# Optimization experiments

Hardware: AMD Instinct MI355X
Metric: run time of the kernel (lower is better)

The kernel has to match this reference:

```python
import jax, jax.numpy as jnp
import numpy as np

N_NODES = 50000
N_EDGES = 800000
NUM_FEATURES = 96
HIDDEN = 96


def _glorot(key, fan_in, fan_out):
    s = np.sqrt(6.0 / (fan_in + fan_out)).astype(np.float32)
    return jax.random.uniform(key, (fan_in, fan_out), minval=-s, maxval=s, dtype=jnp.float32)


def setup_inputs() -> dict:
    key = jax.random.key(0)
    ks = jax.random.split(key, 8)
    x = jax.random.normal(ks[0], (N_NODES, NUM_FEATURES), dtype=jnp.float32)
    edge_index = jax.random.randint(ks[1], (2, N_EDGES), 0, N_NODES, dtype=jnp.int64)
    return {
        "x": x,
        "W1": _glorot(ks[2], NUM_FEATURES, HIDDEN),
        "b1": jnp.zeros((HIDDEN,), jnp.float32),
        "W2": _glorot(ks[3], HIDDEN, HIDDEN),
        "b2": jnp.zeros((HIDDEN,), jnp.float32),
        "W3": _glorot(ks[4], HIDDEN, HIDDEN),
        "b3": jnp.zeros((HIDDEN,), jnp.float32),
        "edge_index": edge_index,
    }


def _gcn_conv(x, src, dst, W, b):
    """PyG GCNConv: add self-loops, symmetric normalization D^-1/2 (A+I) D^-1/2 X W + b."""
    n = x.shape[0]
    h = x @ W  # [N, H]
    # degree with self-loops (in-degree over dst, +1 for the self-loop)
    deg = jax.ops.segment_sum(jnp.ones_like(dst, dtype=h.dtype), dst, num_segments=n) + 1.0
    dinv = jax.lax.rsqrt(deg)  # [N]
    norm = dinv[src] * dinv[dst]  # [E]
    # scatter normalized messages; self-loop contributes h_i / deg_i
    agg = jax.ops.segment_sum(h[src] * norm[:, None], dst, num_segments=n)
    return agg + h * (dinv * dinv)[:, None] + b


def reference(x, W1, b1, W2, b2, W3, b3, edge_index):
    src, dst = edge_index[0], edge_index[1]
    # dropout is a no-op in eval mode (F.dropout with training=False)
    h = jax.nn.relu(_gcn_conv(x, src, dst, W1, b1))
    h = jax.nn.relu(_gcn_conv(h, src, dst, W2, b2))
    return _gcn_conv(h, src, dst, W3, b3)
```

## Files before the change

### kernel.cpp

```cpp
#include <hip/hip_runtime.h>

#define F 96
#define SCAN_B 1024

#define WT_IDX(c, k) ((c) * 96 + (((k) ^ (((c) & 7) << 2))))


__global__ void k_zero_i(int* __restrict__ p, int n) {
    int i = blockIdx.x * blockDim.x + threadIdx.x;
    if (i < n) p[i] = 0;
}

__global__ void k_hist(const int* __restrict__ dst, int* __restrict__ hist, int E) {
    int e = blockIdx.x * blockDim.x + threadIdx.x;
    if (e < E) atomicAdd(&hist[dst[e]], 1);
}

__global__ void k_dinv(const int* __restrict__ hist, float* __restrict__ dinv, int N) {
    int i = blockIdx.x * blockDim.x + threadIdx.x;
    if (i < N) dinv[i] = rsqrtf((float)hist[i] + 1.0f);
}

__global__ __launch_bounds__(SCAN_B) void k_scan1(const int* __restrict__ hist,
                                                  int* __restrict__ incl,
                                                  int* __restrict__ bsum, int N) {
    __shared__ int s[SCAN_B];
    int i = blockIdx.x * SCAN_B + threadIdx.x;
    int v = (i < N) ? hist[i] : 0;
    s[threadIdx.x] = v;
    __syncthreads();
    for (int off = 1; off < SCAN_B; off <<= 1) {
        int add = (threadIdx.x >= off) ? s[threadIdx.x - off] : 0;
        __syncthreads();
        s[threadIdx.x] += add;
        __syncthreads();
    }
    if (i < N) incl[i] = s[threadIdx.x];
    if (threadIdx.x == SCAN_B - 1) bsum[blockIdx.x] = s[SCAN_B - 1];
}

__global__ __launch_bounds__(SCAN_B) void k_scan2(int* __restrict__ bsum, int nb) {
    __shared__ int s[SCAN_B];
    int v = (threadIdx.x < nb) ? bsum[threadIdx.x] : 0;
    s[threadIdx.x] = v;
    __syncthreads();
    for (int off = 1; off < SCAN_B; off <<= 1) {
        int add = (threadIdx.x >= off) ? s[threadIdx.x - off] : 0;
        __syncthreads();
        s[threadIdx.x] += add;
        __syncthreads();
    }
    if (threadIdx.x < nb) bsum[threadIdx.x] = s[threadIdx.x] - v;
}

__global__ void k_scan3(const int* __restrict__ incl, const int* __restrict__ hist,
                        const int* __restrict__ bsum, int* __restrict__ row_ptr,
                        int* __restrict__ cursor, int N, int E) {
    int i = blockIdx.x * blockDim.x + threadIdx.x;
    if (i < N) {
        int start = incl[i] - hist[i] + bsum[i / SCAN_B];
        row_ptr[i] = start;
        cursor[i] = start;
    }
    if (i == 0) row_ptr[N] = E;
}

__global__ void k_place(const int* __restrict__ src, const int* __restrict__ dst,
                        int* __restrict__ cursor, int* __restrict__ csr_src, int E) {
    int e = blockIdx.x * blockDim.x + threadIdx.x;
    if (e >= E) return;
    int pos = atomicAdd(&cursor[dst[e]], 1);
    csr_src[pos] = src[e];
}


template <bool RELU_IN>
__global__ __launch_bounds__(256) void k_dense(const float* __restrict__ X,
                                               const float* __restrict__ W,
                                               float* __restrict__ H, int N) {
    __shared__ float Wt[96 * 96];
    __shared__ float Xs[64][96];
    int t = threadIdx.x;
    for (int i = t; i < F * F; i += 256) {
        int k = i / F, c = i % F;
        Wt[WT_IDX(c, k)] = W[i];
    }
    int row0 = blockIdx.x * 64;
    for (int i = t; i < 64 * 24; i += 256) {
        int r = i / 24, c4 = (i % 24) * 4;
        int gr = row0 + r;
        float4 v = make_float4(0.f, 0.f, 0.f, 0.f);
        if (gr < N) {
            v = *reinterpret_cast<const float4*>(X + (size_t)gr * F + c4);
            if (RELU_IN) {
                v.x = fmaxf(v.x, 0.f); v.y = fmaxf(v.y, 0.f);
                v.z = fmaxf(v.z, 0.f); v.w = fmaxf(v.w, 0.f);
            }
        }
        *reinterpret_cast<float4*>(&Xs[r][c4]) = v;
    }
    __syncthreads();

    int c2 = t & 31;
    int rg = t >> 5;
    float acc[8][3];
#pragma unroll
    for (int j = 0; j < 8; ++j) { acc[j][0] = 0.f; acc[j][1] = 0.f; acc[j][2] = 0.f; }

    for (int k4 = 0; k4 < F; k4 += 4) {
        float4 w0 = *reinterpret_cast<const float4*>(&Wt[WT_IDX(c2, k4)]);
        float4 w1 = *reinterpret_cast<const float4*>(&Wt[WT_IDX(c2 + 32, k4)]);
        float4 w2 = *reinterpret_cast<const float4*>(&Wt[WT_IDX(c2 + 64, k4)]);
#pragma unroll
        for (int j = 0; j < 8; ++j) {
            float4 xv = *reinterpret_cast<const float4*>(&Xs[rg + 8 * j][k4]);
            acc[j][0] = fmaf(xv.x, w0.x, acc[j][0]);
            acc[j][1] = fmaf(xv.x, w1.x, acc[j][1]);
            acc[j][2] = fmaf(xv.x, w2.x, acc[j][2]);
            acc[j][0] = fmaf(xv.y, w0.y, acc[j][0]);
            acc[j][1] = fmaf(xv.y, w1.y, acc[j][1]);
            acc[j][2] = fmaf(xv.y, w2.y, acc[j][2]);
            acc[j][0] = fmaf(xv.z, w0.z, acc[j][0]);
            acc[j][1] = fmaf(xv.z, w1.z, acc[j][1]);
            acc[j][2] = fmaf(xv.z, w2.z, acc[j][2]);
            acc[j][0] = fmaf(xv.w, w0.w, acc[j][0]);
            acc[j][1] = fmaf(xv.w, w1.w, acc[j][1]);
            acc[j][2] = fmaf(xv.w, w2.w, acc[j][2]);
        }
    }

#pragma unroll
    for (int j = 0; j < 8; ++j) {
        int gr = row0 + rg + 8 * j;
        if (gr < N) {
            float* hp = H + (size_t)gr * F;
            hp[c2]      = acc[j][0];
            hp[c2 + 32] = acc[j][1];
            hp[c2 + 64] = acc[j][2];
        }
    }
}


__global__ __launch_bounds__(256) void k_gather(const float* __restrict__ H,
                                                const int* __restrict__ csr_src,
                                                const int* __restrict__ row_ptr,
                                                const float* __restrict__ dinv,
                                                const float* __restrict__ b,
                                                float* __restrict__ O, int N) {
    int t = blockIdx.x * 256 + threadIdx.x;
    int node = t >> 5;
    if (node >= N) return;
    int lf = t & 31;
    int s0 = row_ptr[node], s1 = row_ptr[node + 1];
    float di = dinv[node];
    float d2 = di * di;
    const float* hn = H + (size_t)node * F;
    float a0 = fmaf(hn[lf],      d2, b[lf]);
    float a1 = fmaf(hn[lf + 32], d2, b[lf + 32]);
    float a2 = fmaf(hn[lf + 64], d2, b[lf + 64]);

    int e = s0;
    for (; e + 3 < s1; e += 4) {
        int sA = csr_src[e],     sB = csr_src[e + 1];
        int sC = csr_src[e + 2], sD = csr_src[e + 3];
        float wA = dinv[sA] * di, wB = dinv[sB] * di;
        float wC = dinv[sC] * di, wD = dinv[sD] * di;
        const float* hA = H + (size_t)sA * F;
        const float* hB = H + (size_t)sB * F;
        const float* hC = H + (size_t)sC * F;
        const float* hD = H + (size_t)sD * F;
        a0 = fmaf(hA[lf], wA, a0); a1 = fmaf(hA[lf + 32], wA, a1); a2 = fmaf(hA[lf + 64], wA, a2);
        a0 = fmaf(hB[lf], wB, a0); a1 = fmaf(hB[lf + 32], wB, a1); a2 = fmaf(hB[lf + 64], wB, a2);
        a0 = fmaf(hC[lf], wC, a0); a1 = fmaf(hC[lf + 32], wC, a1); a2 = fmaf(hC[lf + 64], wC, a2);
        a0 = fmaf(hD[lf], wD, a0); a1 = fmaf(hD[lf + 32], wD, a1); a2 = fmaf(hD[lf + 64], wD, a2);
    }
    for (; e < s1; ++e) {
        int sA = csr_src[e];
        float wA = dinv[sA] * di;
        const float* hA = H + (size_t)sA * F;
        a0 = fmaf(hA[lf], wA, a0);
        a1 = fmaf(hA[lf + 32], wA, a1);
        a2 = fmaf(hA[lf + 64], wA, a2);
    }

    float* o = O + (size_t)node * F;
    o[lf]      = a0;
    o[lf + 32] = a1;
    o[lf + 64] = a2;
}


__global__ void k_init_deg(float* __restrict__ deg, int N) {
    int i = blockIdx.x * blockDim.x + threadIdx.x;
    if (i < N) deg[i] = 1.0f;
}
__global__ void k_count(const int* __restrict__ dst, float* __restrict__ deg, int E) {
    int e = blockIdx.x * blockDim.x + threadIdx.x;
    if (e < E) atomicAdd(&deg[dst[e]], 1.0f);
}
__global__ void k_rsqrt(float* __restrict__ deg, int N) {
    int i = blockIdx.x * blockDim.x + threadIdx.x;
    if (i < N) deg[i] = rsqrtf(deg[i]);
}
__global__ void k_init_out(const float* __restrict__ H, const float* __restrict__ dinv,
                           const float* __restrict__ b, float* __restrict__ O, int N) {
    int idx = blockIdx.x * blockDim.x + threadIdx.x;
    if (idx >= N * F) return;
    int i = idx / F, f = idx % F;
    float di = dinv[i];
    O[idx] = fmaf(H[idx], di * di, b[f]);
}
__global__ __launch_bounds__(256) void k_scatter(const float* __restrict__ H,
                                                 const int* __restrict__ src,
                                                 const int* __restrict__ dst,
                                                 const float* __restrict__ dinv,
                                                 float* __restrict__ O, int E) {
    int t = blockIdx.x * 256 + threadIdx.x;
    int e = t >> 5;
    if (e >= E) return;
    int lf = t & 31;
    int s = src[e], d = dst[e];
    float nrm = dinv[s] * dinv[d];
    const float* hs = H + (size_t)s * F;
    float* od = O + (size_t)d * F;
#pragma unroll
    for (int j = 0; j < 3; ++j) atomicAdd(&od[lf + 32 * j], hs[lf + 32 * j] * nrm);
}


extern "C" void kernel_launch(void* const* d_in, const int* in_sizes, int n_in,
                              void* d_out, int out_size, void* d_ws, size_t ws_size,
                              hipStream_t stream) {
    const float* x  = (const float*)d_in[0];
    const float* W1 = (const float*)d_in[1];
    const float* b1 = (const float*)d_in[2];
    const float* W2 = (const float*)d_in[3];
    const float* b2 = (const float*)d_in[4];
    const float* W3 = (const float*)d_in[5];
    const float* b3 = (const float*)d_in[6];
    const int*   ei = (const int*)d_in[7];

    const int N = in_sizes[0] / F;
    const int E = in_sizes[7] / 2;
    const int* src = ei;
    const int* dst = ei + E;
    const size_t NF = (size_t)N * F;

    const int thr = 256;
    dim3 blk(thr);
    int gN  = (N + thr - 1) / thr;
    int gE  = (E + thr - 1) / thr;
    int gDen = (N + 63) / 64;
    int gGat = (int)(((size_t)N * 32 + thr - 1) / thr);
    int nScanB = (N + SCAN_B - 1) / SCAN_B;

    float* dinv    = (float*)d_ws;
    int*   row_ptr = (int*)(dinv + N);
    int*   csr_src = row_ptr + N + 1;
    float* A       = (float*)(csr_src + E);
    float* B       = A + NF;
    int* hist   = (int*)A;
    int* incl   = hist + N;
    int* cursor = (int*)B;
    int* bsum   = cursor + N;

    size_t need = ((size_t)N + (N + 1) + (size_t)E + 2 * NF) * 4;
    float* out = (float*)d_out;

    if (ws_size >= need && nScanB <= SCAN_B) {
        k_zero_i<<<gN, blk, 0, stream>>>(hist, N);
        k_hist<<<gE, blk, 0, stream>>>(dst, hist, E);
        k_scan1<<<nScanB, dim3(SCAN_B), 0, stream>>>(hist, incl, bsum, N);
        k_scan2<<<1, dim3(SCAN_B), 0, stream>>>(bsum, nScanB);
        k_scan3<<<gN, blk, 0, stream>>>(incl, hist, bsum, row_ptr, cursor, N, E);
        k_dinv<<<gN, blk, 0, stream>>>(hist, dinv, N);
        k_place<<<gE, blk, 0, stream>>>(src, dst, cursor, csr_src, E);

        k_dense<false><<<gDen, blk, 0, stream>>>(x, W1, A, N);
        k_gather<<<gGat, blk, 0, stream>>>(A, csr_src, row_ptr, dinv, b1, B, N);
        k_dense<true><<<gDen, blk, 0, stream>>>(B, W2, A, N);
        k_gather<<<gGat, blk, 0, stream>>>(A, csr_src, row_ptr, dinv, b2, B, N);
        k_dense<true><<<gDen, blk, 0, stream>>>(B, W3, A, N);
        k_gather<<<gGat, blk, 0, stream>>>(A, csr_src, row_ptr, dinv, b3, out, N);
    } else {
        float* fdinv = (float*)d_ws;
        float* fA = fdinv + N;
        float* fB = fA + NF;
        int gNF = (int)((NF + thr - 1) / thr);
        int gSc = (int)(((size_t)E * 32 + thr - 1) / thr);
        k_init_deg<<<gN, blk, 0, stream>>>(fdinv, N);
        k_count<<<gE, blk, 0, stream>>>(dst, fdinv, E);
        k_rsqrt<<<gN, blk, 0, stream>>>(fdinv, N);
        k_dense<false><<<gDen, blk, 0, stream>>>(x, W1, fA, N);
        k_init_out<<<gNF, blk, 0, stream>>>(fA, fdinv, b1, fB, N);
        k_scatter<<<gSc, blk, 0, stream>>>(fA, src, dst, fdinv, fB, E);
        k_dense<true><<<gDen, blk, 0, stream>>>(fB, W2, fA, N);
        k_init_out<<<gNF, blk, 0, stream>>>(fA, fdinv, b2, out, N);
        k_scatter<<<gSc, blk, 0, stream>>>(fA, src, dst, fdinv, out, E);
        k_dense<true><<<gDen, blk, 0, stream>>>(out, W3, fA, N);
        k_init_out<<<gNF, blk, 0, stream>>>(fA, fdinv, b3, fB, N);
        k_scatter<<<gSc, blk, 0, stream>>>(fA, src, dst, fdinv, fB, E);
        hipMemcpyAsync(out, fB, NF * sizeof(float), hipMemcpyDeviceToDevice, stream);
    }
}
```

Baseline: 360.9 us.

## Store hidden features in feature-chunked layout and gather per chunk with one thread per node

The dense kernel now writes H as 8 column chunks of 12 features each, every chunk stored contiguously for all nodes. The gather kernel assigns one thread per node per chunk and reads 48-byte vectors, so each chunk's working set is N*48 bytes, which should fit in cache better than the full 384-byte rows. Blocks interleave chunks so that chunks of the same node range run concurrently. Index and output accesses use nontemporal loads and stores. In exchange, the dense stores become scattered, csr_src and dinv are reread once per chunk, and one thread per node may cause load imbalance on high-degree nodes.

```diff
diff --git a/kernel.cpp b/kernel.cpp
--- a/kernel.cpp
+++ b/kernel.cpp
@@ -2,6 +2,10 @@
 
 #define F 96
 #define SCAN_B 1024
+#define CHUNKS 8
+#define CW 12
+
+typedef float f32x4 __attribute__((ext_vector_type(4)));
 
 #define WT_IDX(c, k) ((c) * 96 + (((k) ^ (((c) & 7) << 2))))
 
@@ -74,7 +78,7 @@
 }
 
 
-template <bool RELU_IN>
+template <bool RELU_IN, bool CHUNKED>
 __global__ __launch_bounds__(256) void k_dense(const float* __restrict__ X,
                                                const float* __restrict__ W,
                                                float* __restrict__ H, int N) {
@@ -129,65 +133,111 @@
         }
     }
 
+    size_t NC = (size_t)N * CW;
 #pragma unroll
     for (int j = 0; j < 8; ++j) {
         int gr = row0 + rg + 8 * j;
         if (gr < N) {
-            float* hp = H + (size_t)gr * F;
-            hp[c2]      = acc[j][0];
-            hp[c2 + 32] = acc[j][1];
-            hp[c2 + 64] = acc[j][2];
+            if (CHUNKED) {
+#pragma unroll
+                for (int m = 0; m < 3; ++m) {
+                    int c = c2 + 32 * m;
+                    H[(size_t)(c / CW) * NC + (size_t)gr * CW + (c % CW)] = acc[j][m];
+                }
+            } else {
+                float* hp = H + (size_t)gr * F;
+                hp[c2]      = acc[j][0];
+                hp[c2 + 32] = acc[j][1];
+                hp[c2 + 64] = acc[j][2];
+            }
         }
     }
 }
 
 
-__global__ __launch_bounds__(256) void k_gather(const float* __restrict__ H,
+__global__ __launch_bounds__(256) void k_gather(const float* __restrict__ Hc,
                                                 const int* __restrict__ csr_src,
                                                 const int* __restrict__ row_ptr,
                                                 const float* __restrict__ dinv,
                                                 const float* __restrict__ b,
                                                 float* __restrict__ O, int N) {
-    int t = blockIdx.x * 256 + threadIdx.x;
-    int node = t >> 5;
+    int chunk = blockIdx.x & (CHUNKS - 1);
+    int node = (blockIdx.x >> 3) * 256 + threadIdx.x;
     if (node >= N) return;
-    int lf = t & 31;
-    int s0 = row_ptr[node], s1 = row_ptr[node + 1];
+    size_t NC = (size_t)N * CW;
+    const float* Hk = Hc + (size_t)chunk * NC;
+
+    int s0 = __builtin_nontemporal_load(row_ptr + node);
+    int s1 = __builtin_nontemporal_load(row_ptr + node + 1);
     float di = dinv[node];
     float d2 = di * di;
-    const float* hn = H + (size_t)node * F;
-    float a0 = fmaf(hn[lf],      d2, b[lf]);
-    float a1 = fmaf(hn[lf + 32], d2, b[lf + 32]);
-    float a2 = fmaf(hn[lf + 64], d2, b[lf + 64]);
+
+    const float* bc = b + chunk * CW;
+    const float* hn = Hk + (size_t)node * CW;
+    float4 a0 = *reinterpret_cast<const float4*>(bc);
+    float4 a1 = *reinterpret_cast<const float4*>(bc + 4);
+    float4 a2 = *reinterpret_cast<const float4*>(bc + 8);
+    {
+        float4 h0 = *reinterpret_cast<const float4*>(hn);
+        float4 h1 = *reinterpret_cast<const float4*>(hn + 4);
+        float4 h2 = *reinterpret_cast<const float4*>(hn + 8);
+        a0.x = fmaf(h0.x, d2, a0.x); a0.y = fmaf(h0.y, d2, a0.y);
+        a0.z = fmaf(h0.z, d2, a0.z); a0.w = fmaf(h0.w, d2, a0.w);
+        a1.x = fmaf(h1.x, d2, a1.x); a1.y = fmaf(h1.y, d2, a1.y);
+        a1.z = fmaf(h1.z, d2, a1.z); a1.w = fmaf(h1.w, d2, a1.w);
+        a2.x = fmaf(h2.x, d2, a2.x); a2.y = fmaf(h2.y, d2, a2.y);
+        a2.z = fmaf(h2.z, d2, a2.z); a2.w = fmaf(h2.w, d2, a2.w);
+    }
 
     int e = s0;
-    for (; e + 3 < s1; e += 4) {
-        int sA = csr_src[e],     sB = csr_src[e + 1];
-        int sC = csr_src[e + 2], sD = csr_src[e + 3];
-        float wA = dinv[sA] * di, wB = dinv[sB] * di;
-        float wC = dinv[sC] * di, wD = dinv[sD] * di;
-        const float* hA = H + (size_t)sA * F;
-        const float* hB = H + (size_t)sB * F;
-        const float* hC = H + (size_t)sC * F;
-        const float* hD = H + (size_t)sD * F;
-        a0 = fmaf(hA[lf], wA, a0); a1 = fmaf(hA[lf + 32], wA, a1); a2 = fmaf(hA[lf + 64], wA, a2);
-        a0 = fmaf(hB[lf], wB, a0); a1 = fmaf(hB[lf + 32], wB, a1); a2 = fmaf(hB[lf + 64], wB, a2);
-        a0 = fmaf(hC[lf], wC, a0); a1 = fmaf(hC[lf + 32], wC, a1); a2 = fmaf(hC[lf + 64], wC, a2);
-        a0 = fmaf(hD[lf], wD, a0); a1 = fmaf(hD[lf + 32], wD, a1); a2 = fmaf(hD[lf + 64], wD, a2);
-    }
-    for (; e < s1; ++e) {
-        int sA = csr_src[e];
+    for (; e + 1 < s1; e += 2) {
+        int sA = __builtin_nontemporal_load(csr_src + e);
+        int sB = __builtin_nontemporal_load(csr_src + e + 1);
         float wA = dinv[sA] * di;
-        const float* hA = H + (size_t)sA * F;
-        a0 = fmaf(hA[lf], wA, a0);
-        a1 = fmaf(hA[lf + 32], wA, a1);
-        a2 = fmaf(hA[lf + 64], wA, a2);
-    }
-
-    float* o = O + (size_t)node * F;
-    o[lf]      = a0;
-    o[lf + 32] = a1;
-    o[lf + 64] = a2;
+        float wB = dinv[sB] * di;
+        const float* hA = Hk + (size_t)sA * CW;
+        const float* hB = Hk + (size_t)sB * CW;
+        float4 A0 = *reinterpret_cast<const float4*>(hA);
+        float4 A1 = *reinterpret_cast<const float4*>(hA + 4);
+        float4 A2 = *reinterpret_cast<const float4*>(hA + 8);
+        float4 B0 = *reinterpret_cast<const float4*>(hB);
+        float4 B1 = *reinterpret_cast<const float4*>(hB + 4);
+        float4 B2 = *reinterpret_cast<const float4*>(hB + 8);
+        a0.x = fmaf(A0.x, wA, a0.x); a0.y = fmaf(A0.y, wA, a0.y);
+        a0.z = fmaf(A0.z, wA, a0.z); a0.w = fmaf(A0.w, wA, a0.w);
+        a1.x = fmaf(A1.x, wA, a1.x); a1.y = fmaf(A1.y, wA, a1.y);
+        a1.z = fmaf(A1.z, wA, a1.z); a1.w = fmaf(A1.w, wA, a1.w);
+        a2.x = fmaf(A2.x, wA, a2.x); a2.y = fmaf(A2.y, wA, a2.y);
+        a2.z = fmaf(A2.z, wA, a2.z); a2.w = fmaf(A2.w, wA, a2.w);
+        a0.x = fmaf(B0.x, wB, a0.x); a0.y = fmaf(B0.y, wB, a0.y);
+        a0.z = fmaf(B0.z, wB, a0.z); a0.w = fmaf(B0.w, wB, a0.w);
+        a1.x = fmaf(B1.x, wB, a1.x); a1.y = fmaf(B1.y, wB, a1.y);
+        a1.z = fmaf(B1.z, wB, a1.z); a1.w = fmaf(B1.w, wB, a1.w);
+        a2.x = fmaf(B2.x, wB, a2.x); a2.y = fmaf(B2.y, wB, a2.y);
+        a2.z = fmaf(B2.z, wB, a2.z); a2.w = fmaf(B2.w, wB, a2.w);
+    }
+    if (e < s1) {
+        int sA = __builtin_nontemporal_load(csr_src + e);
+        float wA = dinv[sA] * di;
+        const float* hA = Hk + (size_t)sA * CW;
+        float4 A0 = *reinterpret_cast<const float4*>(hA);
+        float4 A1 = *reinterpret_cast<const float4*>(hA + 4);
+        float4 A2 = *reinterpret_cast<const float4*>(hA + 8);
+        a0.x = fmaf(A0.x, wA, a0.x); a0.y = fmaf(A0.y, wA, a0.y);
+        a0.z = fmaf(A0.z, wA, a0.z); a0.w = fmaf(A0.w, wA, a0.w);
+        a1.x = fmaf(A1.x, wA, a1.x); a1.y = fmaf(A1.y, wA, a1.y);
+        a1.z = fmaf(A1.z, wA, a1.z); a1.w = fmaf(A1.w, wA, a1.w);
+        a2.x = fmaf(A2.x, wA, a2.x); a2.y = fmaf(A2.y, wA, a2.y);
+        a2.z = fmaf(A2.z, wA, a2.z); a2.w = fmaf(A2.w, wA, a2.w);
+    }
+
+    float* o = O + (size_t)node * F + chunk * CW;
+    f32x4 v0 = {a0.x, a0.y, a0.z, a0.w};
+    f32x4 v1 = {a1.x, a1.y, a1.z, a1.w};
+    f32x4 v2 = {a2.x, a2.y, a2.z, a2.w};
+    __builtin_nontemporal_store(v0, (f32x4*)o);
+    __builtin_nontemporal_store(v1, (f32x4*)(o + 4));
+    __builtin_nontemporal_store(v2, (f32x4*)(o + 8));
 }
 
 
@@ -252,7 +302,7 @@
     int gN  = (N + thr - 1) / thr;
     int gE  = (E + thr - 1) / thr;
     int gDen = (N + 63) / 64;
-    int gGat = (int)(((size_t)N * 32 + thr - 1) / thr);
+    int gGat = CHUNKS * ((N + thr - 1) / thr);
     int nScanB = (N + SCAN_B - 1) / SCAN_B;
 
     float* dinv    = (float*)d_ws;
@@ -277,11 +327,11 @@
         k_dinv<<<gN, blk, 0, stream>>>(hist, dinv, N);
         k_place<<<gE, blk, 0, stream>>>(src, dst, cursor, csr_src, E);
 
-        k_dense<false><<<gDen, blk, 0, stream>>>(x, W1, A, N);
+        k_dense<false, true><<<gDen, blk, 0, stream>>>(x, W1, A, N);
         k_gather<<<gGat, blk, 0, stream>>>(A, csr_src, row_ptr, dinv, b1, B, N);
-        k_dense<true><<<gDen, blk, 0, stream>>>(B, W2, A, N);
+        k_dense<true, true><<<gDen, blk, 0, stream>>>(B, W2, A, N);
         k_gather<<<gGat, blk, 0, stream>>>(A, csr_src, row_ptr, dinv, b2, B, N);
-        k_dense<true><<<gDen, blk, 0, stream>>>(B, W3, A, N);
+        k_dense<true, true><<<gDen, blk, 0, stream>>>(B, W3, A, N);
         k_gather<<<gGat, blk, 0, stream>>>(A, csr_src, row_ptr, dinv, b3, out, N);
     } else {
         float* fdinv = (float*)d_ws;
@@ -292,13 +342,13 @@
         k_init_deg<<<gN, blk, 0, stream>>>(fdinv, N);
         k_count<<<gE, blk, 0, stream>>>(dst, fdinv, E);
         k_rsqrt<<<gN, blk, 0, stream>>>(fdinv, N);
-        k_dense<false><<<gDen, blk, 0, stream>>>(x, W1, fA, N);
+        k_dense<false, false><<<gDen, blk, 0, stream>>>(x, W1, fA, N);
         k_init_out<<<gNF, blk, 0, stream>>>(fA, fdinv, b1, fB, N);
         k_scatter<<<gSc, blk, 0, stream>>>(fA, src, dst, fdinv, fB, E);
-        k_dense<true><<<gDen, blk, 0, stream>>>(fB, W2, fA, N);
+        k_dense<true, false><<<gDen, blk, 0, stream>>>(fB, W2, fA, N);
         k_init_out<<<gNF, blk, 0, stream>>>(fA, fdinv, b2, out, N);
         k_scatter<<<gSc, blk, 0, stream>>>(fA, src, dst, fdinv, out, E);
-        k_dense<true><<<gDen, blk, 0, stream>>>(out, W3, fA, N);
+        k_dense<true, false><<<gDen, blk, 0, stream>>>(out, W3, fA, N);
         k_init_out<<<gNF, blk, 0, stream>>>(fA, fdinv, b3, fB, N);
         k_scatter<<<gSc, blk, 0, stream>>>(fA, src, dst, fdinv, fB, E);
         hipMemcpyAsync(out, fB, NF * sizeof(float), hipMemcpyDeviceToDevice, stream);
```

Result: slower. 620.5 us (+71.9%).

## Store features in 8 column-chunked planes so each gather pass fits in cache

Applied to the files above, without the earlier changes.

Intermediate feature matrices are now stored as 8 chunk-major planes of 12 columns, so each gather block handles one chunk over 21 nodes with 12 lanes. This shrinks the working set that random neighbour reads touch to 2.4MB per chunk, which is meant to stay cache-resident instead of thrashing across full 96-wide rows. The dense kernel stages its outputs through shared memory for coalesced float4 writes in either layout. Index loads use nontemporal hints. In exchange, each neighbour read fetches only 48 bytes, row_ptr, csr_src and dinv are re-read once per chunk, and 4 of every 256 threads sit idle.

```diff
diff --git a/kernel.cpp b/kernel.cpp
--- a/kernel.cpp
+++ b/kernel.cpp
@@ -2,6 +2,9 @@
 
 #define F 96
 #define SCAN_B 1024
+#define CHUNKS 8
+#define CW 12
+#define NPB 21
 
 #define WT_IDX(c, k) ((c) * 96 + (((k) ^ (((c) & 7) << 2))))
 
@@ -74,30 +77,50 @@
 }
 
 
-template <bool RELU_IN>
+template <bool RELU_IN, bool CHIN_CHUNK, bool COUT_CHUNK>
 __global__ __launch_bounds__(256) void k_dense(const float* __restrict__ X,
                                                const float* __restrict__ W,
                                                float* __restrict__ H, int N) {
     __shared__ float Wt[96 * 96];
-    __shared__ float Xs[64][96];
+    __shared__ float XsOs[64][100];
     int t = threadIdx.x;
+    const size_t NC = (size_t)N * CW;
+
     for (int i = t; i < F * F; i += 256) {
         int k = i / F, c = i % F;
         Wt[WT_IDX(c, k)] = W[i];
     }
     int row0 = blockIdx.x * 64;
-    for (int i = t; i < 64 * 24; i += 256) {
-        int r = i / 24, c4 = (i % 24) * 4;
-        int gr = row0 + r;
-        float4 v = make_float4(0.f, 0.f, 0.f, 0.f);
-        if (gr < N) {
-            v = *reinterpret_cast<const float4*>(X + (size_t)gr * F + c4);
-            if (RELU_IN) {
-                v.x = fmaxf(v.x, 0.f); v.y = fmaxf(v.y, 0.f);
-                v.z = fmaxf(v.z, 0.f); v.w = fmaxf(v.w, 0.f);
+
+    if (CHIN_CHUNK) {
+        for (int q = t; q < 1536; q += 256) {
+            int f = q / 192, rem = q % 192;
+            int node = rem / 3, o = (rem % 3) * 4;
+            int gr = row0 + node;
+            float4 v = make_float4(0.f, 0.f, 0.f, 0.f);
+            if (gr < N) {
+                v = *reinterpret_cast<const float4*>(X + (size_t)f * NC + (size_t)gr * CW + o);
+                if (RELU_IN) {
+                    v.x = fmaxf(v.x, 0.f); v.y = fmaxf(v.y, 0.f);
+                    v.z = fmaxf(v.z, 0.f); v.w = fmaxf(v.w, 0.f);
+                }
             }
-        }
-        *reinterpret_cast<float4*>(&Xs[r][c4]) = v;
+            *reinterpret_cast<float4*>(&XsOs[node][f * CW + o]) = v;
+        }
+    } else {
+        for (int q = t; q < 1536; q += 256) {
+            int node = q / 24, o = (q % 24) * 4;
+            int gr = row0 + node;
+            float4 v = make_float4(0.f, 0.f, 0.f, 0.f);
+            if (gr < N) {
+                v = *reinterpret_cast<const float4*>(X + (size_t)gr * F + o);
+                if (RELU_IN) {
+                    v.x = fmaxf(v.x, 0.f); v.y = fmaxf(v.y, 0.f);
+                    v.z = fmaxf(v.z, 0.f); v.w = fmaxf(v.w, 0.f);
+                }
+            }
+            *reinterpret_cast<float4*>(&XsOs[node][o]) = v;
+        }
     }
     __syncthreads();
 
@@ -113,7 +136,7 @@
         float4 w2 = *reinterpret_cast<const float4*>(&Wt[WT_IDX(c2 + 64, k4)]);
 #pragma unroll
         for (int j = 0; j < 8; ++j) {
-            float4 xv = *reinterpret_cast<const float4*>(&Xs[rg + 8 * j][k4]);
+            float4 xv = *reinterpret_cast<const float4*>(&XsOs[rg + 8 * j][k4]);
             acc[j][0] = fmaf(xv.x, w0.x, acc[j][0]);
             acc[j][1] = fmaf(xv.x, w1.x, acc[j][1]);
             acc[j][2] = fmaf(xv.x, w2.x, acc[j][2]);
@@ -128,66 +151,87 @@
             acc[j][2] = fmaf(xv.w, w2.w, acc[j][2]);
         }
     }
+    __syncthreads();
 
 #pragma unroll
     for (int j = 0; j < 8; ++j) {
-        int gr = row0 + rg + 8 * j;
-        if (gr < N) {
-            float* hp = H + (size_t)gr * F;
-            hp[c2]      = acc[j][0];
-            hp[c2 + 32] = acc[j][1];
-            hp[c2 + 64] = acc[j][2];
-        }
-    }
-}
-
-
-__global__ __launch_bounds__(256) void k_gather(const float* __restrict__ H,
+        XsOs[rg + 8 * j][c2]      = acc[j][0];
+        XsOs[rg + 8 * j][c2 + 32] = acc[j][1];
+        XsOs[rg + 8 * j][c2 + 64] = acc[j][2];
+    }
+    __syncthreads();
+
+    if (COUT_CHUNK) {
+        for (int q = t; q < 1536; q += 256) {
+            int f = q / 192, rem = q % 192;
+            int node = rem / 3, o = (rem % 3) * 4;
+            int gr = row0 + node;
+            if (gr < N) {
+                *reinterpret_cast<float4*>(H + (size_t)f * NC + (size_t)gr * CW + o) =
+                    *reinterpret_cast<const float4*>(&XsOs[node][f * CW + o]);
+            }
+        }
+    } else {
+        for (int q = t; q < 1536; q += 256) {
+            int node = q / 24, o = (q % 24) * 4;
+            int gr = row0 + node;
+            if (gr < N) {
+                *reinterpret_cast<float4*>(H + (size_t)gr * F + o) =
+                    *reinterpret_cast<const float4*>(&XsOs[node][o]);
+            }
+        }
+    }
+}
+
+
+template <bool OUT_ROW>
+__global__ __launch_bounds__(256) void k_gather(const float* __restrict__ Hc,
                                                 const int* __restrict__ csr_src,
                                                 const int* __restrict__ row_ptr,
                                                 const float* __restrict__ dinv,
                                                 const float* __restrict__ b,
                                                 float* __restrict__ O, int N) {
-    int t = blockIdx.x * 256 + threadIdx.x;
-    int node = t >> 5;
+    int t = threadIdx.x;
+    if (t >= NPB * CW) return;
+    int chunk = blockIdx.x & (CHUNKS - 1);
+    int node = (blockIdx.x >> 3) * NPB + t / CW;
     if (node >= N) return;
-    int lf = t & 31;
-    int s0 = row_ptr[node], s1 = row_ptr[node + 1];
+    int lf = t % CW;
+    size_t NC = (size_t)N * CW;
+    const float* Hk = Hc + (size_t)chunk * NC;
+
+    int s0 = __builtin_nontemporal_load(row_ptr + node);
+    int s1 = __builtin_nontemporal_load(row_ptr + node + 1);
     float di = dinv[node];
-    float d2 = di * di;
-    const float* hn = H + (size_t)node * F;
-    float a0 = fmaf(hn[lf],      d2, b[lf]);
-    float a1 = fmaf(hn[lf + 32], d2, b[lf + 32]);
-    float a2 = fmaf(hn[lf + 64], d2, b[lf + 64]);
+    float acc = fmaf(Hk[(size_t)node * CW + lf], di * di, b[chunk * CW + lf]);
 
     int e = s0;
     for (; e + 3 < s1; e += 4) {
-        int sA = csr_src[e],     sB = csr_src[e + 1];
-        int sC = csr_src[e + 2], sD = csr_src[e + 3];
+        int sA = __builtin_nontemporal_load(csr_src + e);
+        int sB = __builtin_nontemporal_load(csr_src + e + 1);
+        int sC = __builtin_nontemporal_load(csr_src + e + 2);
+        int sD = __builtin_nontemporal_load(csr_src + e + 3);
         float wA = dinv[sA] * di, wB = dinv[sB] * di;
         float wC = dinv[sC] * di, wD = dinv[sD] * di;
-        const float* hA = H + (size_t)sA * F;
-        const float* hB = H + (size_t)sB * F;
-        const float* hC = H + (size_t)sC * F;
-        const float* hD = H + (size_t)sD * F;
-        a0 = fmaf(hA[lf], wA, a0); a1 = fmaf(hA[lf + 32], wA, a1); a2 = fmaf(hA[lf + 64], wA, a2);
-        a0 = fmaf(hB[lf], wB, a0); a1 = fmaf(hB[lf + 32], wB, a1); a2 = fmaf(hB[lf + 64], wB, a2);
-        a0 = fmaf(hC[lf], wC, a0); a1 = fmaf(hC[lf + 32], wC, a1); a2 = fmaf(hC[lf + 64], wC, a2);
-        a0 = fmaf(hD[lf], wD, a0); a1 = fmaf(hD[lf + 32], wD, a1); a2 = fmaf(hD[lf + 64], wD, a2);
+        float hA = Hk[(size_t)sA * CW + lf];
+        float hB = Hk[(size_t)sB * CW + lf];
+        float hC = Hk[(size_t)sC * CW + lf];
+        float hD = Hk[(size_t)sD * CW + lf];
+        acc = fmaf(hA, wA, acc);
+        acc = fmaf(hB, wB, acc);
+        acc = fmaf(hC, wC, acc);
+        acc = fmaf(hD, wD, acc);
     }
     for (; e < s1; ++e) {
-        int sA = csr_src[e];
+        int sA = __builtin_nontemporal_load(csr_src + e);
         float wA = dinv[sA] * di;
-        const float* hA = H + (size_t)sA * F;
-        a0 = fmaf(hA[lf], wA, a0);
-        a1 = fmaf(hA[lf + 32], wA, a1);
-        a2 = fmaf(hA[lf + 64], wA, a2);
-    }
-
-    float* o = O + (size_t)node * F;
-    o[lf]      = a0;
-    o[lf + 32] = a1;
-    o[lf + 64] = a2;
+        acc = fmaf(Hk[(size_t)sA * CW + lf], wA, acc);
+    }
+
+    if (OUT_ROW)
+        O[(size_t)node * F + chunk * CW + lf] = acc;
+    else
+        O[(size_t)chunk * NC + (size_t)node * CW + lf] = acc;
 }
 
 
@@ -252,7 +296,7 @@
     int gN  = (N + thr - 1) / thr;
     int gE  = (E + thr - 1) / thr;
     int gDen = (N + 63) / 64;
-    int gGat = (int)(((size_t)N * 32 + thr - 1) / thr);
+    int gGat = CHUNKS * ((N + NPB - 1) / NPB);
     int nScanB = (N + SCAN_B - 1) / SCAN_B;
 
     float* dinv    = (float*)d_ws;
@@ -277,12 +321,12 @@
         k_dinv<<<gN, blk, 0, stream>>>(hist, dinv, N);
         k_place<<<gE, blk, 0, stream>>>(src, dst, cursor, csr_src, E);
 
-        k_dense<false><<<gDen, blk, 0, stream>>>(x, W1, A, N);
-        k_gather<<<gGat, blk, 0, stream>>>(A, csr_src, row_ptr, dinv, b1, B, N);
-        k_dense<true><<<gDen, blk, 0, stream>>>(B, W2, A, N);
-        k_gather<<<gGat, blk, 0, stream>>>(A, csr_src, row_ptr, dinv, b2, B, N);
-        k_dense<true><<<gDen, blk, 0, stream>>>(B, W3, A, N);
-        k_gather<<<gGat, blk, 0, stream>>>(A, csr_src, row_ptr, dinv, b3, out, N);
+        k_dense<false, false, true><<<gDen, blk, 0, stream>>>(x, W1, A, N);
+        k_gather<false><<<gGat, blk, 0, stream>>>(A, csr_src, row_ptr, dinv, b1, B, N);
+        k_dense<true, true, true><<<gDen, blk, 0, stream>>>(B, W2, A, N);
+        k_gather<false><<<gGat, blk, 0, stream>>>(A, csr_src, row_ptr, dinv, b2, B, N);
+        k_dense<true, true, true><<<gDen, blk, 0, stream>>>(B, W3, A, N);
+        k_gather<true><<<gGat, blk, 0, stream>>>(A, csr_src, row_ptr, dinv, b3, out, N);
     } else {
         float* fdinv = (float*)d_ws;
         float* fA = fdinv + N;
@@ -292,13 +336,13 @@
         k_init_deg<<<gN, blk, 0, stream>>>(fdinv, N);
         k_count<<<gE, blk, 0, stream>>>(dst, fdinv, E);
         k_rsqrt<<<gN, blk, 0, stream>>>(fdinv, N);
-        k_dense<false><<<gDen, blk, 0, stream>>>(x, W1, fA, N);
+        k_dense<false, false, false><<<gDen, blk, 0, stream>>>(x, W1, fA, N);
         k_init_out<<<gNF, blk, 0, stream>>>(fA, fdinv, b1, fB, N);
         k_scatter<<<gSc, blk, 0, stream>>>(fA, src, dst, fdinv, fB, E);
-        k_dense<true><<<gDen, blk, 0, stream>>>(fB, W2, fA, N);
+        k_dense<true, false, false><<<gDen, blk, 0, stream>>>(fB, W2, fA, N);
         k_init_out<<<gNF, blk, 0, stream>>>(fA, fdinv, b2, out, N);
         k_scatter<<<gSc, blk, 0, stream>>>(fA, src, dst, fdinv, out, E);
-        k_dense<true><<<gDen, blk, 0, stream>>>(out, W3, fA, N);
+        k_dense<true, false, false><<<gDen, blk, 0, stream>>>(out, W3, fA, N);
         k_init_out<<<gNF, blk, 0, stream>>>(fA, fdinv, b3, fB, N);
         k_scatter<<<gSc, blk, 0, stream>>>(fA, src, dst, fdinv, fB, E);
         hipMemcpyAsync(out, fB, NF * sizeof(float), hipMemcpyDeviceToDevice, stream);
```

Result: slower. 583.1 us (+61.6%).
